# Optimization experiments

Hardware: AMD Instinct MI355X
Metric: run time of the kernel (lower is better)

Reference implementation:

```python
import jax, jax.numpy as jnp
import numpy as np

B, S, EMBED, FFN, NQ = 8, 4096, 1024, 4096, 8
DIM = 2 ** NQ  # statevector dimension (pennylane wire 0 = most significant bit)


def _cnot_perm(c, t, n):
    """Index permutation for CNOT(control=c, target=t): flip target bit where control bit is 1."""
    idx = np.arange(2 ** n)
    cbit = (idx >> (n - 1 - c)) & 1
    flipped = idx ^ (1 << (n - 1 - t))
    return np.where(cbit == 1, flipped, idx)


# static gate permutations: CNOT chain then ring-closing CNOT
_PERMS = [ _cnot_perm(i, i + 1, NQ) for i in range(NQ - 1) ] + [ _cnot_perm(NQ - 1, 0, NQ) ]
# Z-expectation sign table: signs[q, j] = +1 if bit q of j is 0 else -1  -> [NQ, DIM]
_SIGNS = (1.0 - 2.0 * (((np.arange(DIM)[None, :] >> (NQ - 1 - np.arange(NQ)[:, None])) & 1))).astype(np.float32)


def _apply_rx(state, theta, w):
    """Apply RX(theta) on wire w. state: [T, DIM] complex64, theta: [T]."""
    T = state.shape[0]
    left, right = 2 ** w, 2 ** (NQ - w - 1)
    st = state.reshape(T, left, 2, right)
    c = jnp.cos(theta * 0.5)[:, None, None].astype(jnp.complex64)
    s = (-1j * jnp.sin(theta * 0.5))[:, None, None].astype(jnp.complex64)
    a0, a1 = st[:, :, 0, :], st[:, :, 1, :]
    new = jnp.stack([c * a0 + s * a1, s * a0 + c * a1], axis=2)
    return new.reshape(T, DIM)


def _circuit_expvals(theta):
    """Batched statevector sim of the variational circuit. theta: [T, NQ] -> Z expvals [T, NQ]."""
    T = theta.shape[0]
    state = jnp.zeros((T, DIM), jnp.complex64).at[:, 0].set(1.0)  # |0...0>
    for w in range(NQ):
        state = _apply_rx(state, theta[:, w], w)
    for perm in _PERMS:
        state = state[:, jnp.asarray(perm)]
    probs = jnp.abs(state) ** 2  # [T, DIM] real
    return probs @ jnp.asarray(_SIGNS).T  # [T, NQ]


def setup_inputs() -> dict:
    key = jax.random.key(0)
    k1, k2, k3, k4 = jax.random.split(key, 4)
    x = jax.random.normal(k1, (B, S, EMBED), jnp.float32)
    W_enc = jax.random.normal(k2, (NQ, EMBED), jnp.float32) * (1.0 / np.sqrt(EMBED))
    W_dec = jax.random.normal(k3, (FFN, NQ), jnp.float32) * (1.0 / np.sqrt(NQ))
    W_out = jax.random.normal(k4, (EMBED, FFN), jnp.float32) * (1.0 / np.sqrt(FFN))
    return {"x": x, "W_enc": W_enc, "W_dec": W_dec, "W_out": W_out}


def reference(x, W_enc, W_dec, W_out):
    b, s, _ = x.shape
    theta = jnp.einsum('bse,qe->bsq', x, W_enc).reshape(b * s, NQ)  # encoder -> angles
    z = _circuit_expvals(theta).reshape(b, s, NQ)                   # PauliZ expvals
    h = jax.nn.relu(jnp.einsum('bsq,fq->bsf', z, W_dec))            # decoder + relu
    return jnp.einsum('bsf,ef->bse', h, W_out)                      # out_proj
```

## Files before the change

kernel.cpp:

```cpp
#include <hip/hip_runtime.h>
#include <hip/hip_bf16.h>
#include <stdint.h>

typedef __bf16 bf16;
typedef bf16 bf16x8 __attribute__((ext_vector_type(8)));
typedef bf16 bf16x4 __attribute__((ext_vector_type(4)));
typedef float f32x4 __attribute__((ext_vector_type(4)));

#define NQ_    8
#define EMBED_ 1024
#define FFN_   4096
#define MROWS  32768
#define NOUT   1024
#define NT_    (FFN_ / 64)

__device__ __forceinline__ void gl_lds16(const bf16* g, bf16* l) {
  __builtin_amdgcn_global_load_lds(
      (__attribute__((address_space(1))) void*)(const_cast<bf16*>(g)),
      (__attribute__((address_space(3))) void*)l, 16, 0, 0);
}

#define BAR()   __builtin_amdgcn_s_barrier()
#define VM2()   asm volatile("s_waitcnt vmcnt(2)" ::: "memory")
#define VM0()   asm volatile("s_waitcnt vmcnt(0)" ::: "memory")
#define MFMA(a, b, c) __builtin_amdgcn_mfma_f32_16x16x32_bf16((a), (b), (c), 0, 0, 0)

__global__ __launch_bounds__(256) void k_wcvt(const float* __restrict__ w,
                                              bf16* __restrict__ wb) {
  const int i = (blockIdx.x * 256 + threadIdx.x) * 4;
  const float4 v = *(const float4*)(w + i);
  bf16x4 o;
  o[0] = (bf16)v.x; o[1] = (bf16)v.y; o[2] = (bf16)v.z; o[3] = (bf16)v.w;
  *(bf16x4*)(wb + i) = o;
}

__global__ __launch_bounds__(256) void k_encode(const float* __restrict__ x,
                                                const float* __restrict__ Wenc,
                                                float* __restrict__ z) {
  const int t = threadIdx.x;
  const int wave = t >> 6, lane = t & 63;
  const int r0 = blockIdx.x * 16;

  float4 we[8];
#pragma unroll
  for (int q = 0; q < 8; ++q)
    we[q] = *(const float4*)(Wenc + q * EMBED_ + t * 4);

  __shared__ float red[16][4][8];
  __shared__ float cb[16][8];

  for (int rr = 0; rr < 16; ++rr) {
    const float4 xv = *(const float4*)(x + (size_t)(r0 + rr) * EMBED_ + t * 4);
#pragma unroll
    for (int q = 0; q < 8; ++q) {
      float v = xv.x * we[q].x + xv.y * we[q].y + xv.z * we[q].z + xv.w * we[q].w;
#pragma unroll
      for (int off = 32; off > 0; off >>= 1) v += __shfl_xor(v, off, 64);
      if (lane == 0) red[rr][wave][q] = v;
    }
  }
  __syncthreads();
  if (t < 128) {
    const int rr = t >> 3, q = t & 7;
    const float th = red[rr][0][q] + red[rr][1][q] + red[rr][2][q] + red[rr][3][q];
    cb[rr][q] = cosf(th);
  }
  __syncthreads();
  if (t < 16) {
    float c[8];
#pragma unroll
    for (int q = 0; q < 8; ++q) c[q] = cb[t][q];
    float zz[8];
    zz[0] = c[1] * c[2] * c[3] * c[4] * c[5] * c[6] * c[7];
    float p = c[0];
#pragma unroll
    for (int k = 1; k < 8; ++k) { p *= c[k]; zz[k] = p; }
    float4* zp = (float4*)(z + (size_t)(r0 + t) * 8);
    zp[0] = make_float4(zz[0], zz[1], zz[2], zz[3]);
    zp[1] = make_float4(zz[4], zz[5], zz[6], zz[7]);
  }
}

__global__ __launch_bounds__(256) void k_hgen(const float* __restrict__ z,
                                              const float* __restrict__ Wdec,
                                              bf16* __restrict__ h,
                                              int row0) {
  const int t = threadIdx.x;
  const int f0 = blockIdx.y * 2048 + t * 8;
  const int g0 = row0 + blockIdx.x * 64;
  const int l0 = blockIdx.x * 64;

  float4 wd[16];
#pragma unroll
  for (int i = 0; i < 16; ++i)
    wd[i] = *(const float4*)(Wdec + (size_t)f0 * 8 + i * 4);

  for (int rr = 0; rr < 64; ++rr) {
    const float4* zp = (const float4*)(z + (size_t)(g0 + rr) * 8);
    const float4 z0 = zp[0], z1 = zp[1];
    bf16x8 o;
#pragma unroll
    for (int j = 0; j < 8; ++j) {
      const float4 a = wd[j * 2], b = wd[j * 2 + 1];
      float s = a.x * z0.x + a.y * z0.y + a.z * z0.z + a.w * z0.w +
                b.x * z1.x + b.y * z1.y + b.z * z1.z + b.w * z1.w;
      o[j] = (bf16)fmaxf(s, 0.0f);
    }
    *(bf16x8*)(h + (size_t)(l0 + rr) * FFN_ + f0) = o;
  }
}

__global__ __launch_bounds__(512, 2) void k_gemm8(const bf16* __restrict__ A,
                                                  const bf16* __restrict__ Bt,
                                                  float* __restrict__ C,
                                                  int row0) {
  __shared__ bf16 lds[65536];

  const int nwg = (int)gridDim.x, orig = (int)blockIdx.x;
  const int qd = nwg >> 3, rm = nwg & 7;
  const int xcd = orig & 7;
  const int bid = (xcd < rm ? xcd * (qd + 1) : rm * (qd + 1) + (xcd - rm) * qd) + (orig >> 3);
  const int mi = bid >> 2, ni = bid & 3;

  const int t = threadIdx.x;
  const int wave = t >> 6, lane = t & 63;
  const int wm = wave >> 2, wn = wave & 3;

  const int qrow0 = t >> 3;
  const int qc8 = (t & 7) ^ (qrow0 & 7);
  const int wbase = wave * 512;

  const bf16* gA = A + (size_t)(mi * 256 + qrow0) * FFN_ + qc8 * 8;
  const bf16* gB = Bt + (size_t)(ni * 256 + qrow0) * FFN_ + qc8 * 8;
  const bf16* pA0 = gA;
  const bf16* pA1 = gA + (size_t)64 * FFN_;
  const bf16* pA2 = gA + (size_t)128 * FFN_;
  const bf16* pA3 = gA + (size_t)192 * FFN_;
  const bf16* pB0 = gB;
  const bf16* pB1 = gB + (size_t)64 * FFN_;
  const bf16* pB2 = gB + (size_t)128 * FFN_;
  const bf16* pB3 = gB + (size_t)192 * FFN_;

#define STAGE(p0, p1, roff, ahead, cc)                                          \
  do {                                                                          \
    gl_lds16((p0) + (ahead) * 64, (bf16*)lds + (cc) * 32768 + (roff) + wbase);  \
    gl_lds16((p1) + (ahead) * 64,                                               \
             (bf16*)lds + (cc) * 32768 + (roff) + 4096 + wbase);                \
  } while (0)

  const int fr = lane & 15, fk = (lane >> 4) * 8;
  const int swz = (fr & 7) << 3;
  const int a0 = (wm * 128 + fr) * 64 + (fk ^ swz);
  const int a1 = a0 ^ 32;
  const int b0 = 16384 + (wn * 64 + fr) * 64 + (fk ^ swz);
  const int b1 = b0 ^ 32;

  auto ldA = [&](int c, int m, int kk) -> bf16x8 {
    return *(const bf16x8*)((const bf16*)lds + c * 32768 + (kk ? a1 : a0) + m * 1024);
  };
  auto ldB = [&](int c, int n, int kk) -> bf16x8 {
    return *(const bf16x8*)((const bf16*)lds + c * 32768 + (kk ? b1 : b0) + n * 1024);
  };

  f32x4 acc[8][4] = {};

  STAGE(pA0, pA1, 0, 0, 0);
  STAGE(pA2, pA3, 8192, 0, 0);
  STAGE(pB0, pB1, 16384, 0, 0);
  STAGE(pB2, pB3, 24576, 0, 0);
  STAGE(pA0, pA1, 0, 1, 1);
  VM2();
  BAR();

#pragma unroll 2
  for (int T = 0; T < NT_; ++T) {
    const int c = T & 1, cn = c ^ 1;
    bf16x8 a1r[4][2], a2r[4][2], br[4][2];

#pragma unroll
    for (int m = 0; m < 4; ++m) { a1r[m][0] = ldA(c, m, 0); a1r[m][1] = ldA(c, m, 1); }
#pragma unroll
    for (int n = 0; n < 4; ++n) { br[n][0] = ldB(c, n, 0); br[n][1] = ldB(c, n, 1); }
    if (T + 1 < NT_) STAGE(pB0, pB1, 16384, 1, cn);
    __builtin_amdgcn_s_setprio(1);
#pragma unroll
    for (int m = 0; m < 4; ++m)
#pragma unroll
      for (int n = 0; n < 2; ++n) {
        acc[m][n] = MFMA(a1r[m][0], br[n][0], acc[m][n]);
        acc[m][n] = MFMA(a1r[m][1], br[n][1], acc[m][n]);
      }
    __builtin_amdgcn_s_setprio(0);
    BAR();

    if (T + 1 < NT_) {
      STAGE(pB2, pB3, 24576, 1, cn);
      STAGE(pA2, pA3, 8192, 1, cn);
    }
    __builtin_amdgcn_s_setprio(1);
#pragma unroll
    for (int m = 0; m < 4; ++m)
#pragma unroll
      for (int n = 2; n < 4; ++n) {
        acc[m][n] = MFMA(a1r[m][0], br[n][0], acc[m][n]);
        acc[m][n] = MFMA(a1r[m][1], br[n][1], acc[m][n]);
      }
    __builtin_amdgcn_s_setprio(0);
    BAR();

#pragma unroll
    for (int m = 0; m < 4; ++m) { a2r[m][0] = ldA(c, m + 4, 0); a2r[m][1] = ldA(c, m + 4, 1); }
    __builtin_amdgcn_s_setprio(1);
#pragma unroll
    for (int m = 0; m < 4; ++m)
#pragma unroll
      for (int n = 0; n < 2; ++n) {
        acc[m + 4][n] = MFMA(a2r[m][0], br[n][0], acc[m + 4][n]);
        acc[m + 4][n] = MFMA(a2r[m][1], br[n][1], acc[m + 4][n]);
      }
    __builtin_amdgcn_s_setprio(0);
    BAR();

    if (T + 2 < NT_) STAGE(pA0, pA1, 0, 2, c);
    __builtin_amdgcn_s_setprio(1);
#pragma unroll
    for (int m = 0; m < 4; ++m)
#pragma unroll
      for (int n = 2; n < 4; ++n) {
        acc[m + 4][n] = MFMA(a2r[m][0], br[n][0], acc[m + 4][n]);
        acc[m + 4][n] = MFMA(a2r[m][1], br[n][1], acc[m + 4][n]);
      }
    __builtin_amdgcn_s_setprio(0);
    if (T < NT_ - 2) { VM2(); } else { VM0(); }
    BAR();

    pA0 += 64; pA1 += 64; pA2 += 64; pA3 += 64;
    pB0 += 64; pB1 += 64; pB2 += 64; pB3 += 64;
  }
#undef STAGE

  const int orow = (lane >> 4) * 4, ocol = lane & 15;
  const int rbase = row0 + mi * 256 + wm * 128;
  const int cbase = ni * 256 + wn * 64;
#pragma unroll
  for (int m = 0; m < 8; ++m)
#pragma unroll
    for (int n = 0; n < 4; ++n)
#pragma unroll
      for (int j = 0; j < 4; ++j)
        C[(size_t)(rbase + m * 16 + orow + j) * NOUT + (cbase + n * 16 + ocol)] =
            acc[m][n][j];
}

extern "C" void kernel_launch(void* const* d_in, const int* in_sizes, int n_in,
                              void* d_out, int out_size, void* d_ws, size_t ws_size,
                              hipStream_t stream) {
  const float* x    = (const float*)d_in[0];
  const float* Wenc = (const float*)d_in[1];
  const float* Wdec = (const float*)d_in[2];
  const float* Wout = (const float*)d_in[3];
  float* out = (float*)d_out;

  char* ws = (char*)d_ws;
  bf16*  Wb = (bf16*)ws;
  float* z  = (float*)(ws + 8388608);
  bf16*  h  = (bf16*)(ws + 8388608 + 1048576);

  const size_t head = 8388608 + 1048576;
  const size_t avail = ws_size > head ? ws_size - head : 0;
  int nch = 1;
  while (nch < 128 && (size_t)(MROWS / nch) * FFN_ * 2 > avail) nch <<= 1;
  const int chunk = MROWS / nch;

  k_wcvt<<<4096, 256, 0, stream>>>(Wout, Wb);
  k_encode<<<2048, 256, 0, stream>>>(x, Wenc, z);
  for (int c = 0; c < nch; ++c) {
    const int row0 = c * chunk;
    dim3 hg(chunk / 64, 2);
    k_hgen<<<hg, 256, 0, stream>>>(z, Wdec, h, row0);
    k_gemm8<<<(chunk / 256) * 4, 512, 0, stream>>>(h, Wb, out, row0);
  }
}
```

Measured before the change: 362.4 us.

## Fuse encoder and decoder-ReLU into one kernel; reorder MFMA K-loop

Merges the encoder (x·Wenc, cos products) and the decoder+ReLU h generation into a single kernel that keeps z in shared memory, which removes the z round-trip through global memory and one launch per chunk. Each block now handles 16 rows and reloads Wdec from global memory twice per block, so Wdec is reused across fewer rows than before. The GEMM inner loop also interleaves A/B LDS loads and orders the MFMAs k-slice first, giving more independent accumulator chains between dependent MFMAs.

```diff
diff --git a/kernel.cpp b/kernel.cpp
--- a/kernel.cpp
+++ b/kernel.cpp
@@ -34,12 +34,15 @@
   *(bf16x4*)(wb + i) = o;
 }
 
-__global__ __launch_bounds__(256) void k_encode(const float* __restrict__ x,
-                                                const float* __restrict__ Wenc,
-                                                float* __restrict__ z) {
+__global__ __launch_bounds__(256) void k_fused(const float* __restrict__ x,
+                                               const float* __restrict__ Wenc,
+                                               const float* __restrict__ Wdec,
+                                               bf16* __restrict__ h,
+                                               int row0) {
   const int t = threadIdx.x;
   const int wave = t >> 6, lane = t & 63;
-  const int r0 = blockIdx.x * 16;
+  const int l0 = blockIdx.x * 16;
+  const int r0 = row0 + l0;
 
   float4 we[8];
 #pragma unroll
@@ -48,6 +51,7 @@
 
   __shared__ float red[16][4][8];
   __shared__ float cb[16][8];
+  __shared__ float zs[16][8];
 
   for (int rr = 0; rr < 16; ++rr) {
     const float4 xv = *(const float4*)(x + (size_t)(r0 + rr) * EMBED_ + t * 4);
@@ -70,43 +74,33 @@
     float c[8];
 #pragma unroll
     for (int q = 0; q < 8; ++q) c[q] = cb[t][q];
-    float zz[8];
-    zz[0] = c[1] * c[2] * c[3] * c[4] * c[5] * c[6] * c[7];
+    zs[t][0] = c[1] * c[2] * c[3] * c[4] * c[5] * c[6] * c[7];
     float p = c[0];
 #pragma unroll
-    for (int k = 1; k < 8; ++k) { p *= c[k]; zz[k] = p; }
-    float4* zp = (float4*)(z + (size_t)(r0 + t) * 8);
-    zp[0] = make_float4(zz[0], zz[1], zz[2], zz[3]);
-    zp[1] = make_float4(zz[4], zz[5], zz[6], zz[7]);
-  }
-}
-
-__global__ __launch_bounds__(256) void k_hgen(const float* __restrict__ z,
-                                              const float* __restrict__ Wdec,
-                                              bf16* __restrict__ h,
-                                              int row0) {
-  const int t = threadIdx.x;
-  const int f0 = blockIdx.y * 2048 + t * 8;
-  const int g0 = row0 + blockIdx.x * 64;
-  const int l0 = blockIdx.x * 64;
-
-  float4 wd[16];
-#pragma unroll
-  for (int i = 0; i < 16; ++i)
-    wd[i] = *(const float4*)(Wdec + (size_t)f0 * 8 + i * 4);
-
-  for (int rr = 0; rr < 64; ++rr) {
-    const float4* zp = (const float4*)(z + (size_t)(g0 + rr) * 8);
-    const float4 z0 = zp[0], z1 = zp[1];
-    bf16x8 o;
-#pragma unroll
-    for (int j = 0; j < 8; ++j) {
-      const float4 a = wd[j * 2], b = wd[j * 2 + 1];
-      float s = a.x * z0.x + a.y * z0.y + a.z * z0.z + a.w * z0.w +
-                b.x * z1.x + b.y * z1.y + b.z * z1.z + b.w * z1.w;
-      o[j] = (bf16)fmaxf(s, 0.0f);
+    for (int k = 1; k < 8; ++k) { p *= c[k]; zs[t][k] = p; }
+  }
+  __syncthreads();
+
+#pragma unroll
+  for (int half = 0; half < 2; ++half) {
+    const int f0 = half * 2048 + t * 8;
+    float4 wd[16];
+#pragma unroll
+    for (int i = 0; i < 16; ++i)
+      wd[i] = *(const float4*)(Wdec + (size_t)f0 * 8 + i * 4);
+    for (int rr = 0; rr < 16; ++rr) {
+      const float4 z0 = *(const float4*)(&zs[rr][0]);
+      const float4 z1 = *(const float4*)(&zs[rr][4]);
+      bf16x8 o;
+#pragma unroll
+      for (int j = 0; j < 8; ++j) {
+        const float4 a = wd[j * 2], b = wd[j * 2 + 1];
+        float s = a.x * z0.x + a.y * z0.y + a.z * z0.z + a.w * z0.w +
+                  b.x * z1.x + b.y * z1.y + b.z * z1.z + b.w * z1.w;
+        o[j] = (bf16)fmaxf(s, 0.0f);
+      }
+      *(bf16x8*)(h + (size_t)(l0 + rr) * FFN_ + f0) = o;
     }
-    *(bf16x8*)(h + (size_t)(l0 + rr) * FFN_ + f0) = o;
   }
 }
 
@@ -178,18 +172,18 @@
     bf16x8 a1r[4][2], a2r[4][2], br[4][2];
 
 #pragma unroll
-    for (int m = 0; m < 4; ++m) { a1r[m][0] = ldA(c, m, 0); a1r[m][1] = ldA(c, m, 1); }
-#pragma unroll
-    for (int n = 0; n < 4; ++n) { br[n][0] = ldB(c, n, 0); br[n][1] = ldB(c, n, 1); }
+    for (int m = 0; m < 4; ++m) { a1r[m][0] = ldA(c, m, 0); br[m][0] = ldB(c, m, 0); }
+#pragma unroll
+    for (int m = 0; m < 4; ++m) { a1r[m][1] = ldA(c, m, 1); br[m][1] = ldB(c, m, 1); }
     if (T + 1 < NT_) STAGE(pB0, pB1, 16384, 1, cn);
     __builtin_amdgcn_s_setprio(1);
 #pragma unroll
-    for (int m = 0; m < 4; ++m)
-#pragma unroll
-      for (int n = 0; n < 2; ++n) {
-        acc[m][n] = MFMA(a1r[m][0], br[n][0], acc[m][n]);
-        acc[m][n] = MFMA(a1r[m][1], br[n][1], acc[m][n]);
-      }
+    for (int kk = 0; kk < 2; ++kk)
+#pragma unroll
+      for (int m = 0; m < 4; ++m)
+#pragma unroll
+        for (int n = 0; n < 2; ++n)
+          acc[m][n] = MFMA(a1r[m][kk], br[n][kk], acc[m][n]);
     __builtin_amdgcn_s_setprio(0);
     BAR();
 
@@ -199,12 +193,12 @@
     }
     __builtin_amdgcn_s_setprio(1);
 #pragma unroll
-    for (int m = 0; m < 4; ++m)
-#pragma unroll
-      for (int n = 2; n < 4; ++n) {
-        acc[m][n] = MFMA(a1r[m][0], br[n][0], acc[m][n]);
-        acc[m][n] = MFMA(a1r[m][1], br[n][1], acc[m][n]);
-      }
+    for (int kk = 0; kk < 2; ++kk)
+#pragma unroll
+      for (int m = 0; m < 4; ++m)
+#pragma unroll
+        for (int n = 2; n < 4; ++n)
+          acc[m][n] = MFMA(a1r[m][kk], br[n][kk], acc[m][n]);
     __builtin_amdgcn_s_setprio(0);
     BAR();
 
@@ -212,24 +206,24 @@
     for (int m = 0; m < 4; ++m) { a2r[m][0] = ldA(c, m + 4, 0); a2r[m][1] = ldA(c, m + 4, 1); }
     __builtin_amdgcn_s_setprio(1);
 #pragma unroll
-    for (int m = 0; m < 4; ++m)
-#pragma unroll
-      for (int n = 0; n < 2; ++n) {
-        acc[m + 4][n] = MFMA(a2r[m][0], br[n][0], acc[m + 4][n]);
-        acc[m + 4][n] = MFMA(a2r[m][1], br[n][1], acc[m + 4][n]);
-      }
+    for (int kk = 0; kk < 2; ++kk)
+#pragma unroll
+      for (int m = 0; m < 4; ++m)
+#pragma unroll
+        for (int n = 0; n < 2; ++n)
+          acc[m + 4][n] = MFMA(a2r[m][kk], br[n][kk], acc[m + 4][n]);
     __builtin_amdgcn_s_setprio(0);
     BAR();
 
     if (T + 2 < NT_) STAGE(pA0, pA1, 0, 2, c);
     __builtin_amdgcn_s_setprio(1);
 #pragma unroll
-    for (int m = 0; m < 4; ++m)
-#pragma unroll
-      for (int n = 2; n < 4; ++n) {
-        acc[m + 4][n] = MFMA(a2r[m][0], br[n][0], acc[m + 4][n]);
-        acc[m + 4][n] = MFMA(a2r[m][1], br[n][1], acc[m + 4][n]);
-      }
+    for (int kk = 0; kk < 2; ++kk)
+#pragma unroll
+      for (int m = 0; m < 4; ++m)
+#pragma unroll
+        for (int n = 2; n < 4; ++n)
+          acc[m + 4][n] = MFMA(a2r[m][kk], br[n][kk], acc[m + 4][n]);
     __builtin_amdgcn_s_setprio(0);
     if (T < NT_ - 2) { VM2(); } else { VM0(); }
     BAR();
@@ -263,21 +257,18 @@
 
   char* ws = (char*)d_ws;
   bf16*  Wb = (bf16*)ws;
-  float* z  = (float*)(ws + 8388608);
-  bf16*  h  = (bf16*)(ws + 8388608 + 1048576);
-
-  const size_t head = 8388608 + 1048576;
+  bf16*  h  = (bf16*)(ws + 8388608);
+
+  const size_t head = 8388608;
   const size_t avail = ws_size > head ? ws_size - head : 0;
   int nch = 1;
   while (nch < 128 && (size_t)(MROWS / nch) * FFN_ * 2 > avail) nch <<= 1;
   const int chunk = MROWS / nch;
 
   k_wcvt<<<4096, 256, 0, stream>>>(Wout, Wb);
-  k_encode<<<2048, 256, 0, stream>>>(x, Wenc, z);
   for (int c = 0; c < nch; ++c) {
     const int row0 = c * chunk;
-    dim3 hg(chunk / 64, 2);
-    k_hgen<<<hg, 256, 0, stream>>>(z, Wdec, h, row0);
+    k_fused<<<chunk / 16, 256, 0, stream>>>(x, Wenc, Wdec, h, row0);
     k_gemm8<<<(chunk / 256) * 4, 512, 0, stream>>>(h, Wb, out, row0);
   }
 }
```

Measured after the change: 583.0 us. 60.9% more time.
